# Kernel tuning notes

Measured on AMD Instinct MI355X. Metric: run time of the kernel, lower is better.

Reference implementation:

```python
import jax, jax.numpy as jnp
import numpy as np

B, S, E = 2, 2048, 1024
NH, NKV = 16, 4
HD = E // NH
GS = NH // NKV


def setup_inputs() -> dict:
    key = jax.random.key(0)
    ks = jax.random.split(key, 8)
    sc = 0.02
    query = jax.random.normal(ks[0], (B, S, E), dtype=jnp.float32)
    key_t = jax.random.normal(ks[1], (B, S, E), dtype=jnp.float32)
    value = jax.random.normal(ks[2], (B, S, E), dtype=jnp.float32)
    # causal mask, broadcast shape [1,1,S,S] as in source (unsqueeze(0).unsqueeze(0))
    attn_mask = jnp.tril(jnp.ones((S, S), dtype=bool))[None, None]
    Wq = jax.random.normal(ks[3], (NH * HD, E), dtype=jnp.float32) * sc
    Wk = jax.random.normal(ks[4], (NKV * HD, E), dtype=jnp.float32) * sc
    Wv = jax.random.normal(ks[5], (NKV * HD, E), dtype=jnp.float32) * sc
    Wo = jax.random.normal(ks[6], (E, NH * HD), dtype=jnp.float32) * sc
    return {"query": query, "key": key_t, "value": value, "attn_mask": attn_mask,
            "Wq": Wq, "Wk": Wk, "Wv": Wv, "Wo": Wo}


def reference(query, key, value, attn_mask, Wq, Wk, Wv, Wo):
    # projections (nn.Linear, bias=False: y = x @ W.T)
    q = (query @ Wq.T).reshape(B, S, NH, HD).transpose(0, 2, 1, 3)   # [B,NH,S,HD]
    k = (key @ Wk.T).reshape(B, S, NKV, HD).transpose(0, 2, 1, 3)    # [B,NKV,S,HD]
    v = (value @ Wv.T).reshape(B, S, NKV, HD).transpose(0, 2, 1, 3)  # [B,NKV,S,HD]
    # repeat_interleave over head dim to match query heads
    k = jnp.repeat(k, GS, axis=1)  # [B,NH,S,HD]
    v = jnp.repeat(v, GS, axis=1)
    scale = 1.0 / np.sqrt(HD).astype(np.float32)
    scores = jnp.einsum('bhqd,bhkd->bhqk', q, k) * scale  # [B,NH,S,S]
    scores = jnp.where(attn_mask, scores, -jnp.inf)
    weights = jax.nn.softmax(scores, axis=-1)
    out = jnp.einsum('bhqk,bhkd->bhqd', weights, v)        # [B,NH,S,HD]
    out = out.transpose(0, 2, 1, 3).reshape(B, S, NH * HD)
    return out @ Wo.T  # [B,S,E]
```

## Files before the change

kernel.cpp:

```cpp
#include <hip/hip_runtime.h>
#include <hip/hip_bf16.h>

typedef __attribute__((ext_vector_type(8))) short bf16x8;
typedef __attribute__((ext_vector_type(4))) float f32x4;

#define MFMA16(a, b, c) __builtin_amdgcn_mfma_f32_16x16x32_bf16((a), (b), (c), 0, 0, 0)
#define ASYNC16(g, l)                                                     \
    __builtin_amdgcn_global_load_lds(                                     \
        (const __attribute__((address_space(1))) void*)(g),               \
        (__attribute__((address_space(3))) void*)(l), 16, 0, 0)

constexpr int B_ = 2, S_ = 2048, E_ = 1024, NH_ = 16, NKV_ = 4, HD_ = 64;

__global__ __launch_bounds__(256) void cvt_all(
    const float* __restrict__ s0, const float* __restrict__ s1,
    const float* __restrict__ s2, const float* __restrict__ s3,
    const float* __restrict__ s4, const float* __restrict__ s5,
    const float* __restrict__ s6,
    __hip_bfloat16* __restrict__ d0, __hip_bfloat16* __restrict__ d1,
    __hip_bfloat16* __restrict__ d2, __hip_bfloat16* __restrict__ d3,
    __hip_bfloat16* __restrict__ d4, __hip_bfloat16* __restrict__ d5,
    __hip_bfloat16* __restrict__ d6)
{
    const float* s;
    __hip_bfloat16* d;
    int nb;
    switch (blockIdx.y) {
        case 0: s = s0; d = d0; nb = 2048; break;
        case 1: s = s1; d = d1; nb = 2048; break;
        case 2: s = s2; d = d2; nb = 2048; break;
        case 3: s = s3; d = d3; nb = 512;  break;
        case 4: s = s4; d = d4; nb = 512;  break;
        case 5: s = s5; d = d5; nb = 128;  break;
        default: s = s6; d = d6; nb = 128; break;
    }
    if ((int)blockIdx.x >= nb) return;
    const size_t i = ((size_t)blockIdx.x * 256 + threadIdx.x) * 8;
    const float4 f0 = *reinterpret_cast<const float4*>(s + i);
    const float4 f1 = *reinterpret_cast<const float4*>(s + i + 4);
    union { __hip_bfloat16 h[8]; uint4 u; } t;
    t.h[0] = __float2bfloat16(f0.x); t.h[1] = __float2bfloat16(f0.y);
    t.h[2] = __float2bfloat16(f0.z); t.h[3] = __float2bfloat16(f0.w);
    t.h[4] = __float2bfloat16(f1.x); t.h[5] = __float2bfloat16(f1.y);
    t.h[6] = __float2bfloat16(f1.z); t.h[7] = __float2bfloat16(f1.w);
    *reinterpret_cast<uint4*>(d + i) = t.u;
}

__device__ __forceinline__ void gemm_core(
    const __hip_bfloat16* __restrict__ A,
    const __hip_bfloat16* __restrict__ W,
    void* __restrict__ C,
    const int N, const int mode, const int m0, const int n0,
    __hip_bfloat16* sA, __hip_bfloat16* sW)
{
    const int tid  = threadIdx.x;
    const int l    = tid & 63;
    const int w    = tid >> 6;
    const int quad = l >> 4;
    const int lan  = l & 15;
    const int wm   = (w >> 1) * 64;
    const int wn   = (w & 1) * 64;

    const int srow  = w * 8 + (l >> 3);
    const int scolL = (l & 7) * 8;
    const int scolG = ((l & 7) ^ (l >> 3)) * 8;

    f32x4 acc[4][4] = {};

#define STAGE(buf, kb)                                                    \
    {                                                                     \
        _Pragma("unroll")                                                 \
        for (int q = 0; q < 4; ++q) {                                     \
            const int r_ = q * 32 + srow;                                 \
            ASYNC16(A + (size_t)(m0 + r_) * E_ + (kb) + scolG,            \
                    sA + (buf) * 8192 + r_ * 64 + scolL);                 \
            ASYNC16(W + (size_t)(n0 + r_) * E_ + (kb) + scolG,            \
                    sW + (buf) * 8192 + r_ * 64 + scolL);                 \
        }                                                                 \
    }

    STAGE(0, 0)
    int cur = 0;
#pragma unroll 1
    for (int t = 0; t < 16; ++t) {
        __syncthreads();
        if (t < 15) STAGE(cur ^ 1, (t + 1) * 64)

#pragma unroll
        for (int kk = 0; kk < 2; ++kk) {
            bf16x8 af[4], bf[4];
            const int ca = ((kk * 4 + quad) ^ (lan & 7)) * 8;
#pragma unroll
            for (int i = 0; i < 4; ++i)
                af[i] = *reinterpret_cast<const bf16x8*>(
                    sA + cur * 8192 + (wm + i * 16 + lan) * 64 + ca);
#pragma unroll
            for (int j = 0; j < 4; ++j)
                bf[j] = *reinterpret_cast<const bf16x8*>(
                    sW + cur * 8192 + (wn + j * 16 + lan) * 64 + ca);
#pragma unroll
            for (int i = 0; i < 4; ++i)
#pragma unroll
                for (int j = 0; j < 4; ++j)
                    acc[i][j] = MFMA16(af[i], bf[j], acc[i][j]);
        }
        cur ^= 1;
    }
#undef STAGE

#pragma unroll
    for (int i = 0; i < 4; ++i)
#pragma unroll
        for (int j = 0; j < 4; ++j)
#pragma unroll
            for (int r = 0; r < 4; ++r) {
                const int gm = m0 + wm + i * 16 + quad * 4 + r;
                const int gn = n0 + wn + j * 16 + lan;
                const float v = acc[i][j][r];
                if (mode == 2) {
                    ((float*)C)[(size_t)gm * N + gn] = v;
                } else {
                    const __hip_bfloat16 hv = __float2bfloat16(v);
                    if (mode == 0)
                        ((__hip_bfloat16*)C)[(size_t)gm * N + gn] = hv;
                    else
                        ((__hip_bfloat16*)C)
                            [((size_t)(gm >> 11) * N + gn) * (size_t)S_ +
                             (gm & 2047)] = hv;
                }
            }
}

__global__ __launch_bounds__(256) void gemm_qkv(
    const __hip_bfloat16* __restrict__ qb, const __hip_bfloat16* __restrict__ kb,
    const __hip_bfloat16* __restrict__ vb, const __hip_bfloat16* __restrict__ Wqb,
    const __hip_bfloat16* __restrict__ Wkb, const __hip_bfloat16* __restrict__ Wvb,
    __hip_bfloat16* __restrict__ QO, __hip_bfloat16* __restrict__ Kws,
    __hip_bfloat16* __restrict__ VT)
{
    __shared__ __hip_bfloat16 sA[2 * 8192];
    __shared__ __hip_bfloat16 sW[2 * 8192];
    int id = blockIdx.x;
    const __hip_bfloat16 *A, *W;
    void* C;
    int N, mode, bx, by;
    if (id < 256)      { A = qb; W = Wqb; C = QO;  N = 1024; mode = 0; bx = id & 7; by = id >> 3; }
    else if (id < 320) { id -= 256; A = kb; W = Wkb; C = Kws; N = 256; mode = 0; bx = id & 1; by = id >> 1; }
    else               { id -= 320; A = vb; W = Wvb; C = VT;  N = 256; mode = 1; bx = id & 1; by = id >> 1; }
    gemm_core(A, W, C, N, mode, by * 128, bx * 128, sA, sW);
}

__global__ __launch_bounds__(256) void gemm_out(
    const __hip_bfloat16* __restrict__ QO, const __hip_bfloat16* __restrict__ Wob,
    float* __restrict__ out)
{
    __shared__ __hip_bfloat16 sA[2 * 8192];
    __shared__ __hip_bfloat16 sW[2 * 8192];
    const int id = blockIdx.x;
    gemm_core(QO, Wob, out, 1024, 2, (id >> 3) * 128, (id & 7) * 128, sA, sW);
}

__global__ __launch_bounds__(256) void attn(
    __hip_bfloat16* QO,
    const __hip_bfloat16* __restrict__ Kp,
    const __hip_bfloat16* __restrict__ VT)
{
    __shared__ __hip_bfloat16 sK[64][72];
    __shared__ __hip_bfloat16 sV[64][72];
    __shared__ __hip_bfloat16 sP[4][16][68];

    const int bx   = blockIdx.x;
    const int h    = blockIdx.y;
    const int b    = blockIdx.z;
    const int hk   = h >> 2;
    const int tid  = threadIdx.x;
    const int l    = tid & 63;
    const int w    = tid >> 6;
    const int quad = l >> 4;
    const int lan  = l & 15;
    const float KSC = 0.125f * 1.44269504088896340736f;

    const int kr = tid >> 2;
    const int kc = (tid & 3) * 16;
    const __hip_bfloat16* kg =
        Kp + ((size_t)((b * S_ + kr) * NKV_) + hk) * HD_ + kc;
    const __hip_bfloat16* vg =
        VT + ((size_t)((b * NKV_ + hk) * HD_) + kr) * S_ + kc;
    const size_t kstride = (size_t)64 * NKV_ * HD_;

    for (int half = 0; half < 2; ++half) {
        const int qt  = half ? (31 - bx) : bx;
        const int qr0 = qt * 64 + w * 16;

        const __hip_bfloat16* qp =
            QO + ((size_t)((b * S_ + qr0 + lan) * NH_) + h) * HD_ + quad * 8;
        const bf16x8 aq0 = *reinterpret_cast<const bf16x8*>(qp);
        const bf16x8 aq1 = *reinterpret_cast<const bf16x8*>(qp + 32);

        float m_i[4], l_i[4];
        f32x4 acc_o[4] = {};
#pragma unroll
        for (int r = 0; r < 4; ++r) { m_i[r] = -3.0e38f; l_i[r] = 0.f; }

        uint4 kv0 = *reinterpret_cast<const uint4*>(kg);
        uint4 kv1 = *reinterpret_cast<const uint4*>(kg + 8);
        uint4 vv0 = *reinterpret_cast<const uint4*>(vg);
        uint4 vv1 = *reinterpret_cast<const uint4*>(vg + 8);

        for (int kt = 0; kt <= qt; ++kt) {
            __syncthreads();
            *reinterpret_cast<uint4*>(&sK[kr][kc])     = kv0;
            *reinterpret_cast<uint4*>(&sK[kr][kc + 8]) = kv1;
            *reinterpret_cast<uint4*>(&sV[kr][kc])     = vv0;
            *reinterpret_cast<uint4*>(&sV[kr][kc + 8]) = vv1;
            __syncthreads();

            if (kt < qt) {
                const __hip_bfloat16* kn = kg + (size_t)(kt + 1) * kstride;
                const __hip_bfloat16* vn = vg + (size_t)(kt + 1) * 64;
                kv0 = *reinterpret_cast<const uint4*>(kn);
                kv1 = *reinterpret_cast<const uint4*>(kn + 8);
                vv0 = *reinterpret_cast<const uint4*>(vn);
                vv1 = *reinterpret_cast<const uint4*>(vn + 8);
            }

            f32x4 accs[4] = {};
#pragma unroll
            for (int j = 0; j < 4; ++j) {
                bf16x8 bk0 = *reinterpret_cast<const bf16x8*>(&sK[j * 16 + lan][quad * 8]);
                accs[j] = MFMA16(aq0, bk0, accs[j]);
                bf16x8 bk1 = *reinterpret_cast<const bf16x8*>(&sK[j * 16 + lan][32 + quad * 8]);
                accs[j] = MFMA16(aq1, bk1, accs[j]);
            }

            if (kt == qt) {
#pragma unroll
                for (int j = 0; j < 4; ++j)
#pragma unroll
                    for (int r = 0; r < 4; ++r) {
                        const int qr  = qr0 + quad * 4 + r;
                        const int kcg = kt * 64 + j * 16 + lan;
                        if (kcg > qr) accs[j][r] = -1e30f;
                    }
            }

            float mnew[4], alpha[4], rs[4];
#pragma unroll
            for (int r = 0; r < 4; ++r) {
                float v = fmaxf(fmaxf(accs[0][r], accs[1][r]), fmaxf(accs[2][r], accs[3][r]));
                v = fmaxf(v, __shfl_xor(v, 1));
                v = fmaxf(v, __shfl_xor(v, 2));
                v = fmaxf(v, __shfl_xor(v, 4));
                v = fmaxf(v, __shfl_xor(v, 8));
                mnew[r]  = fmaxf(m_i[r], v);
                alpha[r] = exp2f((m_i[r] - mnew[r]) * KSC);
                rs[r]    = 0.f;
            }
#pragma unroll
            for (int j = 0; j < 4; ++j)
#pragma unroll
                for (int r = 0; r < 4; ++r) {
                    const float p = exp2f((accs[j][r] - mnew[r]) * KSC);
                    rs[r] += p;
                    sP[w][quad * 4 + r][j * 16 + lan] = __float2bfloat16(p);
                }
#pragma unroll
            for (int r = 0; r < 4; ++r) {
                float v = rs[r];
                v += __shfl_xor(v, 1);
                v += __shfl_xor(v, 2);
                v += __shfl_xor(v, 4);
                v += __shfl_xor(v, 8);
                l_i[r] = l_i[r] * alpha[r] + v;
                m_i[r] = mnew[r];
            }
#pragma unroll
            for (int j = 0; j < 4; ++j)
#pragma unroll
                for (int r = 0; r < 4; ++r)
                    acc_o[j][r] *= alpha[r];

            __syncthreads();

#pragma unroll
            for (int kk = 0; kk < 2; ++kk) {
                bf16x8 ap = *reinterpret_cast<const bf16x8*>(&sP[w][lan][kk * 32 + quad * 8]);
#pragma unroll
                for (int j = 0; j < 4; ++j) {
                    bf16x8 bv = *reinterpret_cast<const bf16x8*>(&sV[j * 16 + lan][kk * 32 + quad * 8]);
                    acc_o[j] = MFMA16(ap, bv, acc_o[j]);
                }
            }
        }

#pragma unroll
        for (int j = 0; j < 4; ++j)
#pragma unroll
            for (int r = 0; r < 4; ++r) {
                const int qr = qr0 + quad * 4 + r;
                const float v = acc_o[j][r] / l_i[r];
                QO[((size_t)((b * S_ + qr) * NH_) + h) * HD_ + j * 16 + lan] =
                    __float2bfloat16(v);
            }
    }
}

extern "C" void kernel_launch(void* const* d_in, const int* in_sizes, int n_in,
                              void* d_out, int out_size, void* d_ws, size_t ws_size,
                              hipStream_t stream) {
    const float* q  = (const float*)d_in[0];
    const float* k  = (const float*)d_in[1];
    const float* v  = (const float*)d_in[2];
    const float* Wq = (const float*)d_in[4];
    const float* Wk = (const float*)d_in[5];
    const float* Wv = (const float*)d_in[6];
    const float* Wo = (const float*)d_in[7];

    __hip_bfloat16* ws = (__hip_bfloat16*)d_ws;
    __hip_bfloat16* qb   = ws;
    __hip_bfloat16* kb   = qb  + 4194304;
    __hip_bfloat16* vb   = kb  + 4194304;
    __hip_bfloat16* QO   = vb  + 4194304;
    __hip_bfloat16* Kws  = QO  + 4194304;
    __hip_bfloat16* VT   = Kws + 1048576;
    __hip_bfloat16* Wqb  = VT  + 1048576;
    __hip_bfloat16* Wob  = Wqb + 1048576;
    __hip_bfloat16* Wkb  = Wob + 1048576;
    __hip_bfloat16* Wvb  = Wkb + 262144;

    cvt_all<<<dim3(2048, 7), 256, 0, stream>>>(
        q, k, v, Wq, Wo, Wk, Wv, qb, kb, vb, Wqb, Wob, Wkb, Wvb);

    gemm_qkv<<<dim3(384), 256, 0, stream>>>(
        qb, kb, vb, Wqb, Wkb, Wvb, QO, Kws, VT);

    attn<<<dim3(16, NH_, B_), 256, 0, stream>>>(QO, Kws, VT);

    gemm_out<<<dim3(256), 256, 0, stream>>>(QO, Wob, (float*)d_out);
}
```

Before: 246.6 us.

## Transpose attention MFMAs so P stays in registers via ds_bpermute

Swaps the MFMA operand order so S^T is computed, which puts each lane's accumulator values on a single query row. Softmax reductions then shrink to two cross-lane shuffles over one row, and the P tile is repacked into the B-operand layout with ds_bpermute instead of going through shared memory. This drops the sP buffer and one __syncthreads per key tile. Output stores become packed 8-byte writes. The cost is extra bpermute traffic and per-lane select logic in the inner loop.

Measured after the change: 220.5 us. 10.6% less time.

```diff
diff --git a/kernel.cpp b/kernel.cpp
--- a/kernel.cpp
+++ b/kernel.cpp
@@ -167,7 +167,6 @@
 {
     __shared__ __hip_bfloat16 sK[64][72];
     __shared__ __hip_bfloat16 sV[64][72];
-    __shared__ __hip_bfloat16 sP[4][16][68];
 
     const int bx   = blockIdx.x;
     const int h    = blockIdx.y;
@@ -178,7 +177,11 @@
     const int w    = tid >> 6;
     const int quad = l >> 4;
     const int lan  = l & 15;
+    const bool hi  = quad >= 2;
     const float KSC = 0.125f * 1.44269504088896340736f;
+
+    const int idxA = (((quad & 1) * 32) + lan) * 4;
+    const int idxB = idxA + 64;
 
     const int kr = tid >> 2;
     const int kc = (tid & 3) * 16;
@@ -191,16 +194,15 @@
     for (int half = 0; half < 2; ++half) {
         const int qt  = half ? (31 - bx) : bx;
         const int qr0 = qt * 64 + w * 16;
+        const int qme = qr0 + lan;
 
         const __hip_bfloat16* qp =
-            QO + ((size_t)((b * S_ + qr0 + lan) * NH_) + h) * HD_ + quad * 8;
+            QO + ((size_t)((b * S_ + qme) * NH_) + h) * HD_ + quad * 8;
         const bf16x8 aq0 = *reinterpret_cast<const bf16x8*>(qp);
         const bf16x8 aq1 = *reinterpret_cast<const bf16x8*>(qp + 32);
 
-        float m_i[4], l_i[4];
+        float m_i = -3.0e38f, l_i = 0.f;
         f32x4 acc_o[4] = {};
-#pragma unroll
-        for (int r = 0; r < 4; ++r) { m_i[r] = -3.0e38f; l_i[r] = 0.f; }
 
         uint4 kv0 = *reinterpret_cast<const uint4*>(kg);
         uint4 kv1 = *reinterpret_cast<const uint4*>(kg + 8);
@@ -228,9 +230,9 @@
 #pragma unroll
             for (int j = 0; j < 4; ++j) {
                 bf16x8 bk0 = *reinterpret_cast<const bf16x8*>(&sK[j * 16 + lan][quad * 8]);
-                accs[j] = MFMA16(aq0, bk0, accs[j]);
+                accs[j] = MFMA16(bk0, aq0, accs[j]);
                 bf16x8 bk1 = *reinterpret_cast<const bf16x8*>(&sK[j * 16 + lan][32 + quad * 8]);
-                accs[j] = MFMA16(aq1, bk1, accs[j]);
+                accs[j] = MFMA16(bk1, aq1, accs[j]);
             }
 
             if (kt == qt) {
@@ -238,70 +240,81 @@
                 for (int j = 0; j < 4; ++j)
 #pragma unroll
                     for (int r = 0; r < 4; ++r) {
-                        const int qr  = qr0 + quad * 4 + r;
-                        const int kcg = kt * 64 + j * 16 + lan;
-                        if (kcg > qr) accs[j][r] = -1e30f;
+                        const int kcg = kt * 64 + j * 16 + quad * 4 + r;
+                        if (kcg > qme) accs[j][r] = -1e30f;
                     }
             }
 
-            float mnew[4], alpha[4], rs[4];
-#pragma unroll
-            for (int r = 0; r < 4; ++r) {
-                float v = fmaxf(fmaxf(accs[0][r], accs[1][r]), fmaxf(accs[2][r], accs[3][r]));
-                v = fmaxf(v, __shfl_xor(v, 1));
-                v = fmaxf(v, __shfl_xor(v, 2));
-                v = fmaxf(v, __shfl_xor(v, 4));
-                v = fmaxf(v, __shfl_xor(v, 8));
-                mnew[r]  = fmaxf(m_i[r], v);
-                alpha[r] = exp2f((m_i[r] - mnew[r]) * KSC);
-                rs[r]    = 0.f;
-            }
+            float tm = accs[0][0];
 #pragma unroll
             for (int j = 0; j < 4; ++j)
 #pragma unroll
+                for (int r = 0; r < 4; ++r) tm = fmaxf(tm, accs[j][r]);
+            tm = fmaxf(tm, __shfl_xor(tm, 16));
+            tm = fmaxf(tm, __shfl_xor(tm, 32));
+            const float mnew  = fmaxf(m_i, tm);
+            const float alpha = exp2f((m_i - mnew) * KSC);
+            float ps = 0.f;
+#pragma unroll
+            for (int j = 0; j < 4; ++j)
+#pragma unroll
                 for (int r = 0; r < 4; ++r) {
-                    const float p = exp2f((accs[j][r] - mnew[r]) * KSC);
-                    rs[r] += p;
-                    sP[w][quad * 4 + r][j * 16 + lan] = __float2bfloat16(p);
-                }
-#pragma unroll
-            for (int r = 0; r < 4; ++r) {
-                float v = rs[r];
-                v += __shfl_xor(v, 1);
-                v += __shfl_xor(v, 2);
-                v += __shfl_xor(v, 4);
-                v += __shfl_xor(v, 8);
-                l_i[r] = l_i[r] * alpha[r] + v;
-                m_i[r] = mnew[r];
-            }
+                    const float p = exp2f((accs[j][r] - mnew) * KSC);
+                    accs[j][r] = p;
+                    ps += p;
+                }
+            ps += __shfl_xor(ps, 16);
+            ps += __shfl_xor(ps, 32);
+            l_i = l_i * alpha + ps;
+            m_i = mnew;
+#pragma unroll
+            for (int dd = 0; dd < 4; ++dd)
+#pragma unroll
+                for (int r = 0; r < 4; ++r) acc_o[dd][r] *= alpha;
+
+            uint pk[4][2];
 #pragma unroll
             for (int j = 0; j < 4; ++j)
 #pragma unroll
-                for (int r = 0; r < 4; ++r)
-                    acc_o[j][r] *= alpha[r];
-
-            __syncthreads();
+                for (int hh = 0; hh < 2; ++hh) {
+                    union { __hip_bfloat16 bh[2]; uint u; } t;
+                    t.bh[0] = __float2bfloat16(accs[j][2 * hh]);
+                    t.bh[1] = __float2bfloat16(accs[j][2 * hh + 1]);
+                    pk[j][hh] = t.u;
+                }
 
 #pragma unroll
             for (int kk = 0; kk < 2; ++kk) {
-                bf16x8 ap = *reinterpret_cast<const bf16x8*>(&sP[w][lan][kk * 32 + quad * 8]);
-#pragma unroll
-                for (int j = 0; j < 4; ++j) {
-                    bf16x8 bv = *reinterpret_cast<const bf16x8*>(&sV[j * 16 + lan][kk * 32 + quad * 8]);
-                    acc_o[j] = MFMA16(ap, bv, acc_o[j]);
+                union { uint u[4]; bf16x8 v; } pb;
+#pragma unroll
+                for (int w2 = 0; w2 < 4; ++w2) {
+                    const int idx = (w2 & 2) ? idxB : idxA;
+                    const uint a = (uint)__builtin_amdgcn_ds_bpermute(
+                        idx, (int)pk[2 * kk][w2 & 1]);
+                    const uint bb = (uint)__builtin_amdgcn_ds_bpermute(
+                        idx, (int)pk[2 * kk + 1][w2 & 1]);
+                    pb.u[w2] = hi ? bb : a;
+                }
+#pragma unroll
+                for (int dd = 0; dd < 4; ++dd) {
+                    bf16x8 av = *reinterpret_cast<const bf16x8*>(
+                        &sV[dd * 16 + lan][kk * 32 + quad * 8]);
+                    acc_o[dd] = MFMA16(av, pb.v, acc_o[dd]);
                 }
             }
         }
 
-#pragma unroll
-        for (int j = 0; j < 4; ++j)
-#pragma unroll
-            for (int r = 0; r < 4; ++r) {
-                const int qr = qr0 + quad * 4 + r;
-                const float v = acc_o[j][r] / l_i[r];
-                QO[((size_t)((b * S_ + qr) * NH_) + h) * HD_ + j * 16 + lan] =
-                    __float2bfloat16(v);
-            }
+        const float inv = 1.0f / l_i;
+        __hip_bfloat16* op =
+            QO + ((size_t)((b * S_ + qme) * NH_) + h) * HD_ + quad * 4;
+#pragma unroll
+        for (int dd = 0; dd < 4; ++dd) {
+            union { __hip_bfloat16 bh[4]; uint2 u; } t;
+#pragma unroll
+            for (int r = 0; r < 4; ++r)
+                t.bh[r] = __float2bfloat16(acc_o[dd][r] * inv);
+            *reinterpret_cast<uint2*>(op + dd * 16) = t.u;
+        }
     }
 }
 
```
